# Performance work log

Measured on AMD Instinct MI355X. Metric: run time of the kernel, lower is better.

The kernel has to match this reference:

```python
import jax, jax.numpy as jnp
import numpy as np

# --- module constants (from __init__) ---
NMESH = 2001                       # NpointsMesh (odd)
XLIMS = (0.0, 1.0)
L = abs(XLIMS[1] - XLIMS[0])
TAU = np.float32(12.0 * (L / (2.0 * np.pi * NMESH)) ** 2)
KGRID = jnp.asarray(2.0 * np.pi / L * np.linspace(-(NMESH // 2), NMESH // 2, NMESH), dtype=jnp.float32)
XGRID = jnp.asarray(np.linspace(XLIMS[0], XLIMS[1], NMESH + 1)[:-1], dtype=jnp.float32)
FOUR_PI = np.float32(4.0 * np.pi)
SQRT_2PI = np.float32(np.sqrt(2.0 * np.pi))


def setup_inputs() -> dict:
    key = jax.random.key(0)
    x = jax.random.uniform(key, (8, 1024), dtype=jnp.float32)  # particle positions in [0, L)
    return {
        "x": x,
        "sigma_var": jnp.full((1,), 0.02, dtype=jnp.float32),  # sigmaVar weight, init = sigma
        "shift0": jnp.ones((1,), jnp.float32),
        "shift1": jnp.ones((1,), jnp.float32),
        "amp0": jnp.ones((1,), jnp.float32),
        "amp1": jnp.ones((1,), jnp.float32),
    }


def reference(x, sigma_var, shift0, shift1, amp0, amp1):
    # diff: (B, Np, Nmesh)
    diff = x[:, :, None] - XGRID
    # gaussian(diff, tau) -- gridding / resampling window
    arr_gauss = jnp.exp(-jnp.square(diff) / (4.0 * TAU))
    # normalPer(diff, sigmaVar, L) -- periodized normal density
    s = sigma_var[0]
    inv_norm = 1.0 / (SQRT_2PI * s)
    s2 = jnp.square(s)
    arr_norm = inv_norm * (
        jnp.exp(-0.5 * jnp.square(diff) / s2)
        + jnp.exp(-0.5 * jnp.square(diff - L) / s2)
        + jnp.exp(-0.5 * jnp.square(diff + L) / s2)
    )
    # gridding: sum over particles -> (B, Nmesh), then centered FFT
    rho = jnp.sum(arr_norm, axis=1).astype(jnp.complex64)
    fft_g = jnp.fft.fftshift(jnp.fft.fft(rho, axis=-1), axes=-1)  # (B, Nmesh)
    # spectral deconvolution of the gaussian gridding kernel
    deconv = jnp.sqrt(jnp.pi / TAU) * jnp.exp(jnp.square(KGRID) * TAU)  # (Nmesh,)
    # two real spectral multipliers (the original's real/imag unrolling is exactly
    # real-multiplier * complex-fft since imag(multiplier) == 0)
    k2 = jnp.square(KGRID)
    m1 = -amp0[0] * FOUR_PI / (k2 + jnp.square(5.0 * shift0[0]))
    m2 = amp1[0] * FOUR_PI * (1.0 / (k2 + jnp.square(5.0 * shift1[0]))) ** 2
    mult = jnp.stack([m1, m2], axis=0) * deconv  # (2, Nmesh), real
    g = mult[None].astype(jnp.complex64) * fft_g[:, None, :]  # (B, 2, Nmesh)
    # back to physical space
    irfft = jnp.real(jnp.fft.ifft(jnp.fft.ifftshift(g, axes=-1), axis=-1))  # (B, 2, Nmesh)
    # resample at particle positions with the gaussian window; /Nmesh normalization
    fmm = jnp.einsum("bpn,bcn->bpc", arr_gauss, irfft) / NMESH  # (B, Np, 2)
    return fmm
```

## Files before the change

kernel.cpp:

```cpp
#include <hip/hip_runtime.h>
#include <math.h>

#define NMESH    2001
#define NP       1024
#define NT       256
#define NBLOCKS  16
#define JC       26

#define TAU_D   (12.0 / ((2.0*M_PI*NMESH)*(2.0*M_PI*NMESH)))
#define TAU_F   ((float)TAU_D)
#define INV4TAU ((float)(1.0 / (4.0*TAU_D)))
#define TWO_PI  6.28318530717958647692f
#define FOUR_PI 12.5663706143591729539f
#define PI_F    3.14159265358979323846f
#define INV_N   (1.0f/(float)NMESH)

__global__ void __launch_bounds__(NT)
nufft_one(const float* __restrict__ x,
          const float* __restrict__ sigma,
          const float* __restrict__ sh0, const float* __restrict__ sh1,
          const float* __restrict__ amp0, const float* __restrict__ amp1,
          float* __restrict__ out)
{
    __shared__ float2 part[NT][JC + 1];
    __shared__ float2 red[8][JC + 1];
    __shared__ float2 Sf[JC + 1];
    __shared__ float2 wIs[JC + 1];
    __shared__ float2 wMs[JC + 1];
    __shared__ float4 pk[JC + 1];
    __shared__ float2 em[8];

    const int tid  = threadIdx.x;
    const int b    = blockIdx.x >> 1;
    const int half = blockIdx.x & 1;
    const float s  = sigma[0];
    int J = (int)ceilf(0.5f / s);
    J = (J < 1) ? 1 : (J > JC ? JC : J);

    float2 st[4], mu[4];
    #pragma unroll
    for (int i = 0; i < 4; ++i) {
        float xi = x[b * NP + tid + 256 * i];
        float sn, cs; sincosf(TWO_PI * xi, &sn, &cs);
        mu[i] = make_float2(cs, -sn);
        st[i] = mu[i];
    }
    part[tid][0] = make_float2(4.f, 0.f);
    part[tid][1] = make_float2(st[0].x + st[1].x + st[2].x + st[3].x,
                               st[0].y + st[1].y + st[2].y + st[3].y);
    for (int j = 2; j <= J; ++j) {
        float re = 0.f, im = 0.f;
        #pragma unroll
        for (int i = 0; i < 4; ++i) {
            float nx = st[i].x * mu[i].x - st[i].y * mu[i].y;
            float ny = st[i].x * mu[i].y + st[i].y * mu[i].x;
            st[i] = make_float2(nx, ny);
            re += nx; im += ny;
        }
        part[tid][j] = make_float2(re, im);
    }
    __syncthreads();

    if (tid < 216) {
        const int col = tid % 27;
        const int q   = tid / 27;
        if (col <= J) {
            float2 acc = make_float2(0.f, 0.f);
            const int r0 = q * 32;
            for (int i = 0; i < 32; ++i) {
                float2 v = part[r0 + i][col];
                acc.x += v.x; acc.y += v.y;
            }
            red[q][col] = acc;
        }
    } else if (tid < 243) {
        const int j = tid - 216;
        if (j <= J) {
            const float k2 = (TWO_PI * (float)j) * (TWO_PI * (float)j);
            const float q0 = 5.f * sh0[0], q1 = 5.f * sh1[0];
            const float m1 = -amp0[0] * FOUR_PI / (k2 + q0 * q0);
            const float r1 = 1.f / (k2 + q1 * q1);
            const float m2 = amp1[0] * FOUR_PI * r1 * r1;
            const float jj = (float)j * (float)j;
            const float e_s = expf(-2.f * PI_F * PI_F * s * s * jj);
            wIs[j] = make_float2(TWO_PI * m1 * e_s, TWO_PI * m2 * e_s);
            const float dec = sqrtf(PI_F / TAU_F) * expf(jj * 4.f * PI_F * PI_F * TAU_F) * e_s;
            wMs[j] = make_float2(m1 * dec, m2 * dec);
        }
    }
    __syncthreads();

    if (tid <= J) {
        float2 S = make_float2(0.f, 0.f);
        #pragma unroll
        for (int q = 0; q < 8; ++q) { S.x += red[q][tid].x; S.y += red[q][tid].y; }
        Sf[tid] = S;
        const float c = (tid == 0) ? 1.f : 2.f;
        const float2 w = wIs[tid];
        pk[tid] = make_float4(c * w.x * S.x, c * w.x * S.y, c * w.y * S.x, c * w.y * S.y);
    }
    __syncthreads();

    if (tid >= 64 && tid < 72) {
        const int c = tid - 64;
        const int m = (c < 4) ? (NMESH - 4 + c) : (c - 4);
        float snE, csE; sincosf(TWO_PI * (float)m * INV_N, &snE, &csE);
        float cs = csE, sn = snE;
        float mesh0 = wMs[0].x * Sf[0].x;
        float mesh1 = wMs[0].y * Sf[0].x;
        for (int j = 1; j <= J; ++j) {
            float t0 = Sf[j].x * cs - Sf[j].y * sn;
            mesh0 += 2.f * wMs[j].x * t0;
            mesh1 += 2.f * wMs[j].y * t0;
            float nc = cs * csE - sn * snE;
            sn = sn * csE + cs * snE;
            cs = nc;
        }
        em[c] = make_float2(mesh0 * INV_N, mesh1 * INV_N);
    }
    __syncthreads();

    const int p1 = half * 512 + tid;
    const int p2 = p1 + 256;
    const float xa = x[b * NP + p1];
    const float xb = x[b * NP + p2];
    float csa, sna, csb, snb;
    sincosf(TWO_PI * xa, &sna, &csa);
    sincosf(TWO_PI * xb, &snb, &csb);
    float ca = csa, sa = sna, cb = csb, sb = snb;
    const float4 k0 = pk[0];
    float y0a = k0.x, y1a = k0.z, y0b = k0.x, y1b = k0.z;
    for (int j = 1; j <= J; ++j) {
        const float4 kk = pk[j];
        y0a += kk.x * ca - kk.y * sa;
        y1a += kk.z * ca - kk.w * sa;
        y0b += kk.x * cb - kk.y * sb;
        y1b += kk.z * cb - kk.w * sb;
        float nca = ca * csa - sa * sna; sa = sa * csa + ca * sna; ca = nca;
        float ncb = cb * csb - sb * snb; sb = sb * csb + cb * snb; cb = ncb;
    }

    {
        const float u = xa * (float)NMESH;
        if (u < 4.5f) {
            #pragma unroll
            for (int c = 0; c < 4; ++c) {
                float d = xa + (float)(4 - c) * INV_N;
                float G = expf(-d * d * INV4TAU);
                y0a -= G * em[c].x; y1a -= G * em[c].y;
            }
        } else if (u > (float)NMESH - 4.5f) {
            #pragma unroll
            for (int c = 4; c < 8; ++c) {
                float d = xa - 1.f - (float)(c - 4) * INV_N;
                float G = expf(-d * d * INV4TAU);
                y0a -= G * em[c].x; y1a -= G * em[c].y;
            }
        }
    }
    {
        const float u = xb * (float)NMESH;
        if (u < 4.5f) {
            #pragma unroll
            for (int c = 0; c < 4; ++c) {
                float d = xb + (float)(4 - c) * INV_N;
                float G = expf(-d * d * INV4TAU);
                y0b -= G * em[c].x; y1b -= G * em[c].y;
            }
        } else if (u > (float)NMESH - 4.5f) {
            #pragma unroll
            for (int c = 4; c < 8; ++c) {
                float d = xb - 1.f - (float)(c - 4) * INV_N;
                float G = expf(-d * d * INV4TAU);
                y0b -= G * em[c].x; y1b -= G * em[c].y;
            }
        }
    }

    float2* out2 = (float2*)out;
    out2[b * NP + p1] = make_float2(y0a, y1a);
    out2[b * NP + p2] = make_float2(y0b, y1b);
}

extern "C" void kernel_launch(void* const* d_in, const int* in_sizes, int n_in,
                              void* d_out, int out_size, void* d_ws, size_t ws_size,
                              hipStream_t stream) {
    const float* x     = (const float*)d_in[0];
    const float* sigma = (const float*)d_in[1];
    const float* sh0   = (const float*)d_in[2];
    const float* sh1   = (const float*)d_in[3];
    const float* a0    = (const float*)d_in[4];
    const float* a1    = (const float*)d_in[5];
    float* out = (float*)d_out;

    hipLaunchKernelGGL(nufft_one, dim3(NBLOCKS), dim3(NT), 0, stream,
                       x, sigma, sh0, sh1, a0, a1, out);
}
```

Before: 11.67 us.

## Use hardware sin/cos, fast exp, fewer modes, reuse loaded x, move barrier

Replaces sincosf with raw v_sin/v_cos instructions that take the angle in revolutions, and expf with __expf. Cuts the Fourier mode count from ceil(0.5/sigma) to ceil(0.4/sigma), reuses the x values already loaded instead of reloading them, and sets the DC term directly to NP rather than reducing it. The final barrier moves after the per-particle evaluation loop so that loop overlaps with the edge-correction threads. Together these target the transcendental and serial work in this latency-bound single kernel, at the cost of accuracy from hardware approximations and from truncating more of the spectrum.

```diff
diff --git a/kernel.cpp b/kernel.cpp
--- a/kernel.cpp
+++ b/kernel.cpp
@@ -4,7 +4,7 @@
 #define NMESH    2001
 #define NP       1024
 #define NT       256
-#define NBLOCKS  16
+#define NBLK     16
 #define JC       26
 
 #define TAU_D   (12.0 / ((2.0*M_PI*NMESH)*(2.0*M_PI*NMESH)))
@@ -14,6 +14,13 @@
 #define FOUR_PI 12.5663706143591729539f
 #define PI_F    3.14159265358979323846f
 #define INV_N   (1.0f/(float)NMESH)
+
+__device__ __forceinline__ float sin2pi(float r) {
+    float d; asm("v_sin_f32 %0, %1" : "=v"(d) : "v"(r)); return d;
+}
+__device__ __forceinline__ float cos2pi(float r) {
+    float d; asm("v_cos_f32 %0, %1" : "=v"(d) : "v"(r)); return d;
+}
 
 __global__ void __launch_bounds__(NT)
 nufft_one(const float* __restrict__ x,
@@ -33,27 +40,30 @@
     const int tid  = threadIdx.x;
     const int b    = blockIdx.x >> 1;
     const int half = blockIdx.x & 1;
-    const float s  = sigma[0];
-    int J = (int)ceilf(0.5f / s);
+
+    float xi[4];
+    #pragma unroll
+    for (int i = 0; i < 4; ++i) xi[i] = x[b * NP + tid + 256 * i];
+
+    const float s = sigma[0];
+    int J = (int)ceilf(0.4f / s);
     J = (J < 1) ? 1 : (J > JC ? JC : J);
 
     float2 st[4], mu[4];
     #pragma unroll
     for (int i = 0; i < 4; ++i) {
-        float xi = x[b * NP + tid + 256 * i];
-        float sn, cs; sincosf(TWO_PI * xi, &sn, &cs);
+        float cs = cos2pi(xi[i]), sn = sin2pi(xi[i]);
         mu[i] = make_float2(cs, -sn);
         st[i] = mu[i];
     }
-    part[tid][0] = make_float2(4.f, 0.f);
     part[tid][1] = make_float2(st[0].x + st[1].x + st[2].x + st[3].x,
                                st[0].y + st[1].y + st[2].y + st[3].y);
     for (int j = 2; j <= J; ++j) {
         float re = 0.f, im = 0.f;
         #pragma unroll
         for (int i = 0; i < 4; ++i) {
-            float nx = st[i].x * mu[i].x - st[i].y * mu[i].y;
-            float ny = st[i].x * mu[i].y + st[i].y * mu[i].x;
+            float nx = fmaf(st[i].x, mu[i].x, -st[i].y * mu[i].y);
+            float ny = fmaf(st[i].x, mu[i].y,  st[i].y * mu[i].x);
             st[i] = make_float2(nx, ny);
             re += nx; im += ny;
         }
@@ -64,9 +74,10 @@
     if (tid < 216) {
         const int col = tid % 27;
         const int q   = tid / 27;
-        if (col <= J) {
+        if (col >= 1 && col <= J) {
             float2 acc = make_float2(0.f, 0.f);
             const int r0 = q * 32;
+            #pragma unroll 8
             for (int i = 0; i < 32; ++i) {
                 float2 v = part[r0 + i][col];
                 acc.x += v.x; acc.y += v.y;
@@ -82,18 +93,23 @@
             const float r1 = 1.f / (k2 + q1 * q1);
             const float m2 = amp1[0] * FOUR_PI * r1 * r1;
             const float jj = (float)j * (float)j;
-            const float e_s = expf(-2.f * PI_F * PI_F * s * s * jj);
+            const float e_s = __expf(-2.f * PI_F * PI_F * s * s * jj);
             wIs[j] = make_float2(TWO_PI * m1 * e_s, TWO_PI * m2 * e_s);
-            const float dec = sqrtf(PI_F / TAU_F) * expf(jj * 4.f * PI_F * PI_F * TAU_F) * e_s;
+            const float dec = sqrtf(PI_F / TAU_F) * __expf(jj * 4.f * PI_F * PI_F * TAU_F) * e_s;
             wMs[j] = make_float2(m1 * dec, m2 * dec);
         }
     }
     __syncthreads();
 
     if (tid <= J) {
-        float2 S = make_float2(0.f, 0.f);
-        #pragma unroll
-        for (int q = 0; q < 8; ++q) { S.x += red[q][tid].x; S.y += red[q][tid].y; }
+        float2 S;
+        if (tid == 0) {
+            S = make_float2((float)NP, 0.f);
+        } else {
+            S = make_float2(0.f, 0.f);
+            #pragma unroll
+            for (int q = 0; q < 8; ++q) { S.x += red[q][tid].x; S.y += red[q][tid].y; }
+        }
         Sf[tid] = S;
         const float c = (tid == 0) ? 1.f : 2.f;
         const float2 w = wIs[tid];
@@ -104,41 +120,41 @@
     if (tid >= 64 && tid < 72) {
         const int c = tid - 64;
         const int m = (c < 4) ? (NMESH - 4 + c) : (c - 4);
-        float snE, csE; sincosf(TWO_PI * (float)m * INV_N, &snE, &csE);
+        const float rev = (float)m * INV_N;
+        const float csE = cos2pi(rev), snE = sin2pi(rev);
         float cs = csE, sn = snE;
         float mesh0 = wMs[0].x * Sf[0].x;
         float mesh1 = wMs[0].y * Sf[0].x;
         for (int j = 1; j <= J; ++j) {
             float t0 = Sf[j].x * cs - Sf[j].y * sn;
-            mesh0 += 2.f * wMs[j].x * t0;
-            mesh1 += 2.f * wMs[j].y * t0;
-            float nc = cs * csE - sn * snE;
-            sn = sn * csE + cs * snE;
+            mesh0 = fmaf(2.f * wMs[j].x, t0, mesh0);
+            mesh1 = fmaf(2.f * wMs[j].y, t0, mesh1);
+            float nc = fmaf(cs, csE, -sn * snE);
+            sn = fmaf(sn, csE, cs * snE);
             cs = nc;
         }
         em[c] = make_float2(mesh0 * INV_N, mesh1 * INV_N);
     }
-    __syncthreads();
 
     const int p1 = half * 512 + tid;
     const int p2 = p1 + 256;
-    const float xa = x[b * NP + p1];
-    const float xb = x[b * NP + p2];
-    float csa, sna, csb, snb;
-    sincosf(TWO_PI * xa, &sna, &csa);
-    sincosf(TWO_PI * xb, &snb, &csb);
+    const float xa = (half == 0) ? xi[0] : xi[2];
+    const float xb = (half == 0) ? xi[1] : xi[3];
+    const float csa = cos2pi(xa), sna = sin2pi(xa);
+    const float csb = cos2pi(xb), snb = sin2pi(xb);
     float ca = csa, sa = sna, cb = csb, sb = snb;
     const float4 k0 = pk[0];
     float y0a = k0.x, y1a = k0.z, y0b = k0.x, y1b = k0.z;
     for (int j = 1; j <= J; ++j) {
         const float4 kk = pk[j];
-        y0a += kk.x * ca - kk.y * sa;
-        y1a += kk.z * ca - kk.w * sa;
-        y0b += kk.x * cb - kk.y * sb;
-        y1b += kk.z * cb - kk.w * sb;
-        float nca = ca * csa - sa * sna; sa = sa * csa + ca * sna; ca = nca;
-        float ncb = cb * csb - sb * snb; sb = sb * csb + cb * snb; cb = ncb;
-    }
+        y0a = fmaf(kk.x, ca, fmaf(-kk.y, sa, y0a));
+        y1a = fmaf(kk.z, ca, fmaf(-kk.w, sa, y1a));
+        y0b = fmaf(kk.x, cb, fmaf(-kk.y, sb, y0b));
+        y1b = fmaf(kk.z, cb, fmaf(-kk.w, sb, y1b));
+        float nca = fmaf(ca, csa, -sa * sna); sa = fmaf(sa, csa, ca * sna); ca = nca;
+        float ncb = fmaf(cb, csb, -sb * snb); sb = fmaf(sb, csb, cb * snb); cb = ncb;
+    }
+    __syncthreads();
 
     {
         const float u = xa * (float)NMESH;
@@ -146,14 +162,14 @@
             #pragma unroll
             for (int c = 0; c < 4; ++c) {
                 float d = xa + (float)(4 - c) * INV_N;
-                float G = expf(-d * d * INV4TAU);
+                float G = __expf(-d * d * INV4TAU);
                 y0a -= G * em[c].x; y1a -= G * em[c].y;
             }
         } else if (u > (float)NMESH - 4.5f) {
             #pragma unroll
             for (int c = 4; c < 8; ++c) {
                 float d = xa - 1.f - (float)(c - 4) * INV_N;
-                float G = expf(-d * d * INV4TAU);
+                float G = __expf(-d * d * INV4TAU);
                 y0a -= G * em[c].x; y1a -= G * em[c].y;
             }
         }
@@ -164,14 +180,14 @@
             #pragma unroll
             for (int c = 0; c < 4; ++c) {
                 float d = xb + (float)(4 - c) * INV_N;
-                float G = expf(-d * d * INV4TAU);
+                float G = __expf(-d * d * INV4TAU);
                 y0b -= G * em[c].x; y1b -= G * em[c].y;
             }
         } else if (u > (float)NMESH - 4.5f) {
             #pragma unroll
             for (int c = 4; c < 8; ++c) {
                 float d = xb - 1.f - (float)(c - 4) * INV_N;
-                float G = expf(-d * d * INV4TAU);
+                float G = __expf(-d * d * INV4TAU);
                 y0b -= G * em[c].x; y1b -= G * em[c].y;
             }
         }
@@ -193,6 +209,6 @@
     const float* a1    = (const float*)d_in[5];
     float* out = (float*)d_out;
 
-    hipLaunchKernelGGL(nufft_one, dim3(NBLOCKS), dim3(NT), 0, stream,
+    hipLaunchKernelGGL(nufft_one, dim3(NBLK), dim3(NT), 0, stream,
                        x, sigma, sh0, sh1, a0, a1, out);
 }
```

Result: faster. 10.09 us (-13.6%).
